# Kernel optimization log

Hardware: AMD Instinct MI355X
Metric: run time of the kernel (lower is better)

Reference implementation:

```python
import jax, jax.numpy as jnp
import numpy as np


def setup_inputs() -> dict:
    key = jax.random.key(0)
    ks = jax.random.split(key, 13)
    HID = 256
    N = 2 * HID                      # hidden_dim * 2
    B_DOC, S, T_K = 32, 40, 64      # docs, sentences/doc, max words/sentence
    B_SENT = B_DOC * S               # total sentences = sum(sent_lens)
    MAX_DOC_LEN = S * T_K
    f = jnp.float32
    sc = jnp.float32(0.05)
    sent_lens = jnp.full((B_DOC,), S, dtype=jnp.int32)
    inp = {
        "s_t_hat": jax.random.normal(ks[0], (B_DOC, N), f),
        "encoder_outputs": jax.random.normal(ks[1], (B_SENT, T_K, N), f),
        "encoder_feature": jax.random.normal(ks[2], (B_SENT * T_K, N), f) * jnp.float32(0.5),
        "seq_lens2": jax.random.randint(ks[3], (B_SENT,), T_K // 2, T_K + 1, dtype=jnp.int32),
        "sent_s_t_hat": jax.random.normal(ks[4], (B_DOC, N), f),
        "sent_enc_outputs": jax.random.normal(ks[5], (B_DOC, S, N), f),
        "sent_enc_feature": jax.random.normal(ks[6], (B_DOC * S, N), f) * jnp.float32(0.5),
        "sent_enc_padding_mask": (jnp.arange(S)[None, :] < sent_lens[:, None]).astype(f),
        "sent_lens": sent_lens,
        "max_doc_len": MAX_DOC_LEN,
        "coverage": jnp.zeros((B_SENT, T_K), f),
        "Wd": jax.random.normal(ks[7], (N, N), f) * sc,
        "bd": jax.random.normal(ks[8], (N,), f) * sc,
        "v_w": jax.random.normal(ks[9], (N,), f) * sc,
        "Wsd": jax.random.normal(ks[10], (N, N), f) * sc,
        "bsd": jax.random.normal(ks[11], (N,), f) * sc,
        "sv_w": jax.random.normal(ks[12], (N,), f) * sc,
    }
    return inp


def _excl_cumsum(x):
    return jnp.cumsum(x) - x


def reference(s_t_hat, encoder_outputs, encoder_feature, seq_lens2, sent_s_t_hat,
              sent_enc_outputs, sent_enc_feature, sent_enc_padding_mask, sent_lens,
              max_doc_len, coverage, Wd, bd, v_w, Wsd, bsd, sv_w):
    B_SENT, T_K, N = encoder_outputs.shape
    B_DOC, S, _ = sent_enc_outputs.shape
    dtype = encoder_outputs.dtype

    # sentence s -> owning doc (replaces first Python loop: broadcast dec_fea per doc)
    doc_ids = jnp.repeat(jnp.arange(B_DOC), sent_lens, total_repeat_length=B_SENT)

    # ---- word-level additive attention over each sentence ----
    dec_fea = s_t_hat @ Wd + bd                              # [B_DOC, N]
    att = jnp.tanh(encoder_feature.reshape(B_SENT, T_K, N) + dec_fea[doc_ids][:, None, :])
    scores = att @ v_w                                        # [B_SENT, T_K]
    w_mask = (jnp.arange(T_K)[None, :] < seq_lens2[:, None]).astype(dtype)
    w_attn_ = jax.nn.softmax(scores, axis=1) * w_mask
    w_attn = w_attn_ / w_attn_.sum(1, keepdims=True)          # [B_SENT, T_K]

    # ---- sentence-level additive attention over each doc ----
    sent_dec_fea = sent_s_t_hat @ Wsd + bsd                   # [B_DOC, N]
    sent_att = jnp.tanh(sent_enc_feature.reshape(B_DOC, S, N) + sent_dec_fea[:, None, :])
    sent_scores = sent_att @ sv_w                             # [B_DOC, S]
    sent_attn_ = jax.nn.softmax(sent_scores, axis=1) * sent_enc_padding_mask
    sent_attn_dist = sent_attn_ / sent_attn_.sum(1, keepdims=True)

    # ---- ragged flatten: scatter valid words of each sentence into its doc stream ----
    sent_start = _excl_cumsum(sent_lens)                      # first sentence idx per doc
    sent_local = jnp.arange(B_SENT) - sent_start[doc_ids]     # sentence pos within doc
    mult_attn = sent_attn_dist[doc_ids, sent_local][:, None] * w_attn  # [B_SENT, T_K]

    word_cum = _excl_cumsum(seq_lens2)                        # global word offsets
    doc_word_off = word_cum - word_cum[sent_start[doc_ids]]   # offset within doc
    pos = doc_word_off[:, None] + jnp.arange(T_K)[None, :]    # [B_SENT, T_K]
    valid = jnp.arange(T_K)[None, :] < seq_lens2[:, None]
    flat = jnp.where(valid, doc_ids[:, None] * max_doc_len + pos, B_DOC * max_doc_len)
    flat = flat.reshape(-1)

    enc_output2 = (jnp.zeros((B_DOC * max_doc_len, N), dtype)
                   .at[flat].set(encoder_outputs.reshape(-1, N), mode="drop")
                   .reshape(B_DOC, max_doc_len, N))
    attn_dist_sw = (jnp.zeros((B_DOC * max_doc_len,), dtype)
                    .at[flat].set(mult_attn.reshape(-1), mode="drop")
                    .reshape(B_DOC, max_doc_len))

    c_t = jnp.einsum("bl,bln->bn", attn_dist_sw, enc_output2)  # [B_DOC, N]
    return (c_t, attn_dist_sw, coverage, sent_attn_dist)
```

## Files before the change

kernel.cpp:

```cpp
#include <hip/hip_runtime.h>
#include <hip/hip_bf16.h>
#include <math.h>

#define B_DOC 32
#define S_MAX 40
#define T_K 64
#define N_DIM 512
#define B_SENT (B_DOC * S_MAX)
#define MAXDOC (S_MAX * T_K)
#define KCHUNK 4

__device__ __forceinline__ float fast_tanh(float x) {
    float e = __expf(2.0f * x);
    return 1.0f - 2.0f * __builtin_amdgcn_rcpf(e + 1.0f);
}

__global__ __launch_bounds__(256) void prep_fea_kernel(
        const int* __restrict__ seq_lens2, const int* __restrict__ sent_lens,
        const float* __restrict__ s_t_hat, const float* __restrict__ sent_s_t_hat,
        const float* __restrict__ Wd, const float* __restrict__ bd,
        const float* __restrict__ Wsd, const float* __restrict__ bsd,
        float* __restrict__ fea_part,
        int* __restrict__ doc_ids, int* __restrict__ sent_local,
        int* __restrict__ doc_word_off, int* __restrict__ sent_start_g,
        int* __restrict__ doc_words_total) {
    int tid = threadIdx.x;
    if (blockIdx.x == 256) {
        __shared__ int ss[B_DOC + 1];
        __shared__ int wc[B_SENT + 1];
        __shared__ int wsum[4];
        int lane = tid & 63, w = tid >> 6;

        int ls[5];
        #pragma unroll
        for (int k = 0; k < 5; ++k) ls[k] = seq_lens2[tid * 5 + k];
        int sum = ls[0] + ls[1] + ls[2] + ls[3] + ls[4];

        int scan = sum;
        #pragma unroll
        for (int off = 1; off < 64; off <<= 1) {
            int v = __shfl_up(scan, off, 64);
            if (lane >= off) scan += v;
        }
        if (lane == 63) wsum[w] = scan;

        if (w == 0) {
            int sl = (lane < B_DOC) ? sent_lens[lane] : 0;
            int sc2 = sl;
            #pragma unroll
            for (int off = 1; off < 64; off <<= 1) {
                int v = __shfl_up(sc2, off, 64);
                if (lane >= off) sc2 += v;
            }
            if (lane < B_DOC) ss[lane + 1] = sc2;
            if (lane == 0) ss[0] = 0;
        }
        __syncthreads();

        int wbase = 0;
        for (int i = 0; i < w; ++i) wbase += wsum[i];
        int excl = wbase + scan - sum;
        #pragma unroll
        for (int k = 0; k < 5; ++k) { wc[tid * 5 + k] = excl; excl += ls[k]; }
        if (tid == 255) wc[B_SENT] = excl;
        __syncthreads();

        if (tid <= B_DOC) sent_start_g[tid] = ss[tid];
        if (tid < B_DOC) doc_words_total[tid] = wc[ss[tid + 1]] - wc[ss[tid]];

        for (int i = tid; i < B_SENT; i += 256) {
            int lo = 0, hi = B_DOC - 1;
            while (lo < hi) { int mid = (lo + hi + 1) >> 1; if (ss[mid] <= i) lo = mid; else hi = mid - 1; }
            doc_ids[i] = lo;
            sent_local[i] = i - ss[lo];
            doc_word_off[i] = wc[i] - wc[ss[lo]];
        }
    } else {
        int blk = blockIdx.x;
        int c = blk & (KCHUNK - 1);
        int b = (blk >> 2) & 31;
        int m = blk >> 7;
        const int KC = N_DIM / KCHUNK;
        const float* x = (m ? sent_s_t_hat : s_t_hat) + b * N_DIM + c * KC;
        const float* W = (m ? Wsd : Wd) + (size_t)c * KC * N_DIM;
        const float* bias = (m ? bsd : bd);
        float* out = fea_part + ((size_t)(m * 32 + b) * KCHUNK + c) * N_DIM;
        __shared__ float xs[128];
        if (tid < KC) xs[tid] = x[tid];
        __syncthreads();
        float a0 = 0.f, a1 = 0.f;
        if (c == 0) { a0 = bias[tid]; a1 = bias[tid + 256]; }
        #pragma unroll 8
        for (int k = 0; k < KC; ++k) {
            float xv = xs[k];
            a0 = fmaf(xv, W[k * N_DIM + tid], a0);
            a1 = fmaf(xv, W[k * N_DIM + tid + 256], a1);
        }
        out[tid] = a0;
        out[tid + 256] = a1;
    }
}

__global__ __launch_bounds__(256) void sent_attn_kernel(
        const float* __restrict__ sef, const float* __restrict__ fea_part,
        const float* __restrict__ sv_w, const float* __restrict__ mask,
        float* __restrict__ out_sent) {
    int b = blockIdx.x;
    __shared__ float df[N_DIM];
    __shared__ float vw[N_DIM];
    __shared__ float sc[S_MAX];
    int tid = threadIdx.x;
    const float* fp = fea_part + (size_t)(32 + b) * KCHUNK * N_DIM;
    for (int i = tid; i < N_DIM; i += 256) {
        df[i] = fp[i] + fp[N_DIM + i] + fp[2 * N_DIM + i] + fp[3 * N_DIM + i];
        vw[i] = sv_w[i];
    }
    __syncthreads();
    int w = tid >> 6, lane = tid & 63;
    const float4* sef4 = (const float4*)(sef + (size_t)b * S_MAX * N_DIM);
    const float4* df4 = (const float4*)df;
    const float4* vw4 = (const float4*)vw;
    for (int t = w; t < S_MAX; t += 4) {
        float acc = 0.0f;
        #pragma unroll
        for (int j = 0; j < 2; ++j) {
            int n4 = lane + 64 * j;
            float4 e = sef4[t * 128 + n4];
            float4 d = df4[n4];
            float4 v = vw4[n4];
            acc = fmaf(v.x, fast_tanh(e.x + d.x), acc);
            acc = fmaf(v.y, fast_tanh(e.y + d.y), acc);
            acc = fmaf(v.z, fast_tanh(e.z + d.z), acc);
            acc = fmaf(v.w, fast_tanh(e.w + d.w), acc);
        }
        #pragma unroll
        for (int off = 32; off >= 1; off >>= 1) acc += __shfl_xor(acc, off, 64);
        if (lane == 0) sc[t] = acc;
    }
    __syncthreads();
    if (tid < 64) {
        bool valid = tid < S_MAX;
        float x = valid ? sc[tid] : -INFINITY;
        float m = x;
        #pragma unroll
        for (int off = 32; off >= 1; off >>= 1) m = fmaxf(m, __shfl_xor(m, off, 64));
        float mk = valid ? mask[b * S_MAX + tid] : 0.0f;
        float e = valid ? __expf(x - m) * mk : 0.0f;
        float ssum = e;
        #pragma unroll
        for (int off = 32; off >= 1; off >>= 1) ssum += __shfl_xor(ssum, off, 64);
        if (valid) out_sent[b * S_MAX + tid] = e / ssum;
    }
}

__global__ __launch_bounds__(256, 4) void fused_kernel(
        const float* __restrict__ ef, const float* __restrict__ eo,
        const float* __restrict__ fea_part, const float* __restrict__ v_w,
        const float* __restrict__ sent_attn, const int* __restrict__ seq_lens2,
        const int* __restrict__ doc_ids, const int* __restrict__ sent_local,
        const int* __restrict__ doc_word_off, const int* __restrict__ sent_start,
        const int* __restrict__ doc_words_total, const int* __restrict__ mdl,
        const float* __restrict__ cov_in,
        float* __restrict__ part, float* __restrict__ out_attn,
        float* __restrict__ out_cov) {
    int s = blockIdx.x;
    int tid = threadIdx.x;
    int w = tid >> 6, lane = tid & 63;
    int h = lane >> 5, sub = lane & 31;
    __shared__ float sc[T_K];
    __shared__ float wl[4];
    __shared__ __align__(16) float4 red[4][128];

    int doc = doc_ids[s];
    int len = seq_lens2[s];
    int maxdoc = mdl[0];

    const float4* fp4 = (const float4*)(fea_part + (size_t)doc * KCHUNK * N_DIM);
    const float4* vw4 = (const float4*)v_w;
    float4 d[4], v[4];
    #pragma unroll
    for (int k = 0; k < 4; ++k) {
        int j = sub + 32 * k;
        float4 a = fp4[j], b = fp4[128 + j], c = fp4[256 + j], e = fp4[384 + j];
        d[k].x = a.x + b.x + c.x + e.x;
        d[k].y = a.y + b.y + c.y + e.y;
        d[k].z = a.z + b.z + c.z + e.z;
        d[k].w = a.w + b.w + c.w + e.w;
        v[k] = vw4[j];
    }

    if (tid < T_K) out_cov[s * T_K + tid] = cov_in[s * T_K + tid];

    const float4* ef4 = (const float4*)ef + (size_t)s * T_K * 128;
    const float4* eo4 = (const float4*)eo + (size_t)s * T_K * 128;

    float l_w = 0.0f;
    float4 O[4];
    #pragma unroll
    for (int k = 0; k < 4; ++k) O[k] = (float4){0.f, 0.f, 0.f, 0.f};

    int t = 2 * w;
    float4 ea[4];
    {
        int row = t + h;
        #pragma unroll
        for (int k = 0; k < 4; ++k) ea[k] = ef4[row * 128 + sub + 32 * k];
    }
    for (; t < len; t += 8) {
        int row = t + h;
        float4 p4[4];
        #pragma unroll
        for (int k = 0; k < 4; ++k) p4[k] = eo4[row * 128 + sub + 32 * k];
        float4 eb[4];
        int tn = t + 8;
        if (tn < len) {
            int rown = tn + h;
            #pragma unroll
            for (int k = 0; k < 4; ++k) eb[k] = ef4[rown * 128 + sub + 32 * k];
        }
        float a0, a1, a2, a3;
        a0  = v[0].x * fast_tanh(ea[0].x + d[0].x);
        a1  = v[1].x * fast_tanh(ea[1].x + d[1].x);
        a2  = v[2].x * fast_tanh(ea[2].x + d[2].x);
        a3  = v[3].x * fast_tanh(ea[3].x + d[3].x);
        a0 = fmaf(v[0].y, fast_tanh(ea[0].y + d[0].y), a0);
        a1 = fmaf(v[1].y, fast_tanh(ea[1].y + d[1].y), a1);
        a2 = fmaf(v[2].y, fast_tanh(ea[2].y + d[2].y), a2);
        a3 = fmaf(v[3].y, fast_tanh(ea[3].y + d[3].y), a3);
        a0 = fmaf(v[0].z, fast_tanh(ea[0].z + d[0].z), a0);
        a1 = fmaf(v[1].z, fast_tanh(ea[1].z + d[1].z), a1);
        a2 = fmaf(v[2].z, fast_tanh(ea[2].z + d[2].z), a2);
        a3 = fmaf(v[3].z, fast_tanh(ea[3].z + d[3].z), a3);
        a0 = fmaf(v[0].w, fast_tanh(ea[0].w + d[0].w), a0);
        a1 = fmaf(v[1].w, fast_tanh(ea[1].w + d[1].w), a1);
        a2 = fmaf(v[2].w, fast_tanh(ea[2].w + d[2].w), a2);
        a3 = fmaf(v[3].w, fast_tanh(ea[3].w + d[3].w), a3);
        float acc = (a0 + a1) + (a2 + a3);
        #pragma unroll
        for (int off = 16; off >= 1; off >>= 1) acc += __shfl_xor(acc, off, 64);
        bool valid = (t + h) < len;
        if (sub == 0 && valid) sc[t + h] = acc;
        float p = valid ? __expf(acc) : 0.0f;
        l_w += p;
        #pragma unroll
        for (int k = 0; k < 4; ++k) {
            O[k].x = fmaf(p, p4[k].x, O[k].x);
            O[k].y = fmaf(p, p4[k].y, O[k].y);
            O[k].z = fmaf(p, p4[k].z, O[k].z);
            O[k].w = fmaf(p, p4[k].w, O[k].w);
        }
        #pragma unroll
        for (int k = 0; k < 4; ++k) ea[k] = eb[k];
    }

    l_w += __shfl_xor(l_w, 32, 64);
    #pragma unroll
    for (int k = 0; k < 4; ++k) {
        O[k].x += __shfl_xor(O[k].x, 32, 64);
        O[k].y += __shfl_xor(O[k].y, 32, 64);
        O[k].z += __shfl_xor(O[k].z, 32, 64);
        O[k].w += __shfl_xor(O[k].w, 32, 64);
    }
    if (lane == 0) wl[w] = l_w;
    if (h == 0) {
        #pragma unroll
        for (int k = 0; k < 4; ++k) red[w][sub + 32 * k] = O[k];
    }
    __syncthreads();

    float l = (wl[0] + wl[1]) + (wl[2] + wl[3]);
    float sa = sent_attn[doc * S_MAX + sent_local[s]];
    float inv = sa / l;
    if (tid < 128) {
        float4 a = red[0][tid], b = red[1][tid], c = red[2][tid], e = red[3][tid];
        float4 r = {(a.x + b.x + c.x + e.x) * inv, (a.y + b.y + c.y + e.y) * inv,
                    (a.z + b.z + c.z + e.z) * inv, (a.w + b.w + c.w + e.w) * inv};
        ((float4*)(part + (size_t)s * N_DIM))[tid] = r;
    }
    if (tid < T_K && tid < len) {
        float mu = sa * __expf(sc[tid]) / l;
        out_attn[(size_t)doc * maxdoc + doc_word_off[s] + tid] = mu;
    }
    if (s + 1 == sent_start[doc + 1]) {
        int dwt = doc_words_total[doc];
        for (int i = dwt + tid; i < maxdoc; i += 256)
            out_attn[(size_t)doc * maxdoc + i] = 0.0f;
    }
}

__global__ __launch_bounds__(128) void reduce_kernel(
        const float* __restrict__ part, const int* __restrict__ sent_start,
        float* __restrict__ c_t) {
    int b = blockIdx.x;
    int nq = threadIdx.x;
    int st = sent_start[b], en = sent_start[b + 1];
    float4 acc = {0.f, 0.f, 0.f, 0.f};
    for (int s = st; s < en; ++s) {
        float4 p = ((const float4*)(part + (size_t)s * N_DIM))[nq];
        acc.x += p.x; acc.y += p.y; acc.z += p.z; acc.w += p.w;
    }
    ((float4*)(c_t + (size_t)b * N_DIM))[nq] = acc;
}

extern "C" void kernel_launch(void* const* d_in, const int* in_sizes, int n_in,
                              void* d_out, int out_size, void* d_ws, size_t ws_size,
                              hipStream_t stream) {
    const float* s_t_hat        = (const float*)d_in[0];
    const float* encoder_out    = (const float*)d_in[1];
    const float* encoder_feat   = (const float*)d_in[2];
    const int*   seq_lens2      = (const int*)d_in[3];
    const float* sent_s_t_hat   = (const float*)d_in[4];
    const float* sent_enc_feat  = (const float*)d_in[6];
    const float* sent_pad_mask  = (const float*)d_in[7];
    const int*   sent_lens      = (const int*)d_in[8];
    const int*   max_doc_len    = (const int*)d_in[9];
    const float* coverage       = (const float*)d_in[10];
    const float* Wd             = (const float*)d_in[11];
    const float* bd             = (const float*)d_in[12];
    const float* v_w            = (const float*)d_in[13];
    const float* Wsd            = (const float*)d_in[14];
    const float* bsd            = (const float*)d_in[15];
    const float* sv_w           = (const float*)d_in[16];

    float* out      = (float*)d_out;
    float* o_ct     = out;
    float* o_attn   = out + B_DOC * N_DIM;
    float* o_cov    = o_attn + B_DOC * MAXDOC;
    float* o_sent   = o_cov + B_SENT * T_K;

    float* ws          = (float*)d_ws;
    float* fea_part    = ws;
    float* part        = ws + 131072;
    int*   ints        = (int*)(ws + 131072 + 655360);
    int*   doc_ids     = ints;
    int*   sent_local  = ints + B_SENT;
    int*   doc_w_off   = ints + 2 * B_SENT;
    int*   sent_start  = ints + 3 * B_SENT;
    int*   doc_wtot    = ints + 3 * B_SENT + 33;

    prep_fea_kernel<<<257, 256, 0, stream>>>(seq_lens2, sent_lens, s_t_hat,
                                             sent_s_t_hat, Wd, bd, Wsd, bsd,
                                             fea_part, doc_ids, sent_local,
                                             doc_w_off, sent_start, doc_wtot);
    sent_attn_kernel<<<B_DOC, 256, 0, stream>>>(sent_enc_feat, fea_part, sv_w,
                                                sent_pad_mask, o_sent);
    fused_kernel<<<B_SENT, 256, 0, stream>>>(encoder_feat, encoder_out, fea_part,
                                             v_w, o_sent, seq_lens2, doc_ids,
                                             sent_local, doc_w_off, sent_start,
                                             doc_wtot, max_doc_len, coverage,
                                             part, o_attn, o_cov);
    reduce_kernel<<<B_DOC, 128, 0, stream>>>(part, sent_start, o_ct);
}
```

Before: 78.04 us.

## Fuse sentence attention into stage-1 kernel and fold reduction via last-block atomics

Merges the sentence-level attention kernel into the preparation kernel: each of 32 extra blocks computes the full Wsd projection for one doc, then the sentence scores and softmax. The separate reduce kernel is removed, and the last block finishing each doc (found with an atomic counter and threadfence) sums the per-sentence partials into c_t. This cuts the launch count from four to two. In exchange, each sentence block does a serial 512-long dot loop, and every block in the main kernel now pays for a fence and an atomic.

```diff
diff --git a/kernel.cpp b/kernel.cpp
--- a/kernel.cpp
+++ b/kernel.cpp
@@ -15,21 +15,45 @@
     return 1.0f - 2.0f * __builtin_amdgcn_rcpf(e + 1.0f);
 }
 
-__global__ __launch_bounds__(256) void prep_fea_kernel(
+__global__ __launch_bounds__(256) void stage1_kernel(
         const int* __restrict__ seq_lens2, const int* __restrict__ sent_lens,
         const float* __restrict__ s_t_hat, const float* __restrict__ sent_s_t_hat,
         const float* __restrict__ Wd, const float* __restrict__ bd,
         const float* __restrict__ Wsd, const float* __restrict__ bsd,
-        float* __restrict__ fea_part,
+        const float* __restrict__ sef, const float* __restrict__ sv_w,
+        const float* __restrict__ mask,
+        float* __restrict__ fea_part, float* __restrict__ o_sent,
         int* __restrict__ doc_ids, int* __restrict__ sent_local,
         int* __restrict__ doc_word_off, int* __restrict__ sent_start_g,
-        int* __restrict__ doc_words_total) {
+        int* __restrict__ doc_words_total, int* __restrict__ cnt) {
     int tid = threadIdx.x;
-    if (blockIdx.x == 256) {
+    int blk = blockIdx.x;
+    if (blk < 128) {
+        int c = blk & (KCHUNK - 1);
+        int b = blk >> 2;
+        const int KC = N_DIM / KCHUNK;
+        const float* x = s_t_hat + b * N_DIM + c * KC;
+        const float* W = Wd + (size_t)c * KC * N_DIM;
+        float* out = fea_part + ((size_t)b * KCHUNK + c) * N_DIM;
+        __shared__ float xs[128];
+        if (tid < KC) xs[tid] = x[tid];
+        __syncthreads();
+        float a0 = 0.f, a1 = 0.f;
+        if (c == 0) { a0 = bd[tid]; a1 = bd[tid + 256]; }
+        #pragma unroll 8
+        for (int k = 0; k < KC; ++k) {
+            float xv = xs[k];
+            a0 = fmaf(xv, W[k * N_DIM + tid], a0);
+            a1 = fmaf(xv, W[k * N_DIM + tid + 256], a1);
+        }
+        out[tid] = a0;
+        out[tid + 256] = a1;
+    } else if (blk == 128) {
         __shared__ int ss[B_DOC + 1];
         __shared__ int wc[B_SENT + 1];
         __shared__ int wsum[4];
         int lane = tid & 63, w = tid >> 6;
+        if (tid < B_DOC) cnt[tid] = 0;
 
         int ls[5];
         #pragma unroll
@@ -76,80 +100,61 @@
             doc_word_off[i] = wc[i] - wc[ss[lo]];
         }
     } else {
-        int blk = blockIdx.x;
-        int c = blk & (KCHUNK - 1);
-        int b = (blk >> 2) & 31;
-        int m = blk >> 7;
-        const int KC = N_DIM / KCHUNK;
-        const float* x = (m ? sent_s_t_hat : s_t_hat) + b * N_DIM + c * KC;
-        const float* W = (m ? Wsd : Wd) + (size_t)c * KC * N_DIM;
-        const float* bias = (m ? bsd : bd);
-        float* out = fea_part + ((size_t)(m * 32 + b) * KCHUNK + c) * N_DIM;
-        __shared__ float xs[128];
-        if (tid < KC) xs[tid] = x[tid];
-        __syncthreads();
-        float a0 = 0.f, a1 = 0.f;
-        if (c == 0) { a0 = bias[tid]; a1 = bias[tid + 256]; }
+        int doc = blk - 129;
+        __shared__ __align__(16) float xs[N_DIM];
+        __shared__ __align__(16) float df[N_DIM];
+        __shared__ __align__(16) float vw[N_DIM];
+        __shared__ float sc[S_MAX];
+        xs[tid] = sent_s_t_hat[doc * N_DIM + tid];
+        xs[tid + 256] = sent_s_t_hat[doc * N_DIM + tid + 256];
+        vw[tid] = sv_w[tid];
+        vw[tid + 256] = sv_w[tid + 256];
+        __syncthreads();
+        float a0 = bsd[tid], a1 = bsd[tid + 256];
         #pragma unroll 8
-        for (int k = 0; k < KC; ++k) {
+        for (int k = 0; k < N_DIM; ++k) {
             float xv = xs[k];
-            a0 = fmaf(xv, W[k * N_DIM + tid], a0);
-            a1 = fmaf(xv, W[k * N_DIM + tid + 256], a1);
-        }
-        out[tid] = a0;
-        out[tid + 256] = a1;
-    }
-}
-
-__global__ __launch_bounds__(256) void sent_attn_kernel(
-        const float* __restrict__ sef, const float* __restrict__ fea_part,
-        const float* __restrict__ sv_w, const float* __restrict__ mask,
-        float* __restrict__ out_sent) {
-    int b = blockIdx.x;
-    __shared__ float df[N_DIM];
-    __shared__ float vw[N_DIM];
-    __shared__ float sc[S_MAX];
-    int tid = threadIdx.x;
-    const float* fp = fea_part + (size_t)(32 + b) * KCHUNK * N_DIM;
-    for (int i = tid; i < N_DIM; i += 256) {
-        df[i] = fp[i] + fp[N_DIM + i] + fp[2 * N_DIM + i] + fp[3 * N_DIM + i];
-        vw[i] = sv_w[i];
-    }
-    __syncthreads();
-    int w = tid >> 6, lane = tid & 63;
-    const float4* sef4 = (const float4*)(sef + (size_t)b * S_MAX * N_DIM);
-    const float4* df4 = (const float4*)df;
-    const float4* vw4 = (const float4*)vw;
-    for (int t = w; t < S_MAX; t += 4) {
-        float acc = 0.0f;
-        #pragma unroll
-        for (int j = 0; j < 2; ++j) {
-            int n4 = lane + 64 * j;
-            float4 e = sef4[t * 128 + n4];
-            float4 d = df4[n4];
-            float4 v = vw4[n4];
-            acc = fmaf(v.x, fast_tanh(e.x + d.x), acc);
-            acc = fmaf(v.y, fast_tanh(e.y + d.y), acc);
-            acc = fmaf(v.z, fast_tanh(e.z + d.z), acc);
-            acc = fmaf(v.w, fast_tanh(e.w + d.w), acc);
-        }
-        #pragma unroll
-        for (int off = 32; off >= 1; off >>= 1) acc += __shfl_xor(acc, off, 64);
-        if (lane == 0) sc[t] = acc;
-    }
-    __syncthreads();
-    if (tid < 64) {
-        bool valid = tid < S_MAX;
-        float x = valid ? sc[tid] : -INFINITY;
-        float m = x;
-        #pragma unroll
-        for (int off = 32; off >= 1; off >>= 1) m = fmaxf(m, __shfl_xor(m, off, 64));
-        float mk = valid ? mask[b * S_MAX + tid] : 0.0f;
-        float e = valid ? __expf(x - m) * mk : 0.0f;
-        float ssum = e;
-        #pragma unroll
-        for (int off = 32; off >= 1; off >>= 1) ssum += __shfl_xor(ssum, off, 64);
-        if (valid) out_sent[b * S_MAX + tid] = e / ssum;
+            a0 = fmaf(xv, Wsd[k * N_DIM + tid], a0);
+            a1 = fmaf(xv, Wsd[k * N_DIM + tid + 256], a1);
+        }
+        df[tid] = a0;
+        df[tid + 256] = a1;
+        __syncthreads();
+        int g = tid >> 5, sub = tid & 31;
+        const float4* df4 = (const float4*)df;
+        const float4* vw4 = (const float4*)vw;
+        for (int r = g; r < S_MAX; r += 8) {
+            const float4* row = (const float4*)(sef + ((size_t)doc * S_MAX + r) * N_DIM);
+            float acc = 0.0f;
+            #pragma unroll
+            for (int k = 0; k < 4; ++k) {
+                int j = sub + 32 * k;
+                float4 e = row[j];
+                float4 d = df4[j];
+                float4 v = vw4[j];
+                acc = fmaf(v.x, fast_tanh(e.x + d.x), acc);
+                acc = fmaf(v.y, fast_tanh(e.y + d.y), acc);
+                acc = fmaf(v.z, fast_tanh(e.z + d.z), acc);
+                acc = fmaf(v.w, fast_tanh(e.w + d.w), acc);
+            }
+            #pragma unroll
+            for (int off = 16; off >= 1; off >>= 1) acc += __shfl_xor(acc, off, 32);
+            if (sub == 0) sc[r] = acc;
+        }
+        __syncthreads();
+        if (tid < 64) {
+            bool valid = tid < S_MAX;
+            float x = valid ? sc[tid] : -INFINITY;
+            float m = x;
+            #pragma unroll
+            for (int off = 32; off >= 1; off >>= 1) m = fmaxf(m, __shfl_xor(m, off, 64));
+            float mk = valid ? mask[doc * S_MAX + tid] : 0.0f;
+            float e = valid ? __expf(x - m) * mk : 0.0f;
+            float ssum = e;
+            #pragma unroll
+            for (int off = 32; off >= 1; off >>= 1) ssum += __shfl_xor(ssum, off, 64);
+            if (valid) o_sent[doc * S_MAX + tid] = e / ssum;
+        }
     }
 }
 
@@ -162,7 +167,8 @@
         const int* __restrict__ doc_words_total, const int* __restrict__ mdl,
         const float* __restrict__ cov_in,
         float* __restrict__ part, float* __restrict__ out_attn,
-        float* __restrict__ out_cov) {
+        float* __restrict__ out_cov, float* __restrict__ c_t,
+        int* __restrict__ cnt) {
     int s = blockIdx.x;
     int tid = threadIdx.x;
     int w = tid >> 6, lane = tid & 63;
@@ -170,6 +176,7 @@
     __shared__ float sc[T_K];
     __shared__ float wl[4];
     __shared__ __align__(16) float4 red[4][128];
+    __shared__ int isLast;
 
     int doc = doc_ids[s];
     int len = seq_lens2[s];
@@ -281,25 +288,30 @@
         float mu = sa * __expf(sc[tid]) / l;
         out_attn[(size_t)doc * maxdoc + doc_word_off[s] + tid] = mu;
     }
-    if (s + 1 == sent_start[doc + 1]) {
+    int st = sent_start[doc], en = sent_start[doc + 1];
+    if (s + 1 == en) {
         int dwt = doc_words_total[doc];
         for (int i = dwt + tid; i < maxdoc; i += 256)
             out_attn[(size_t)doc * maxdoc + i] = 0.0f;
     }
-}
-
-__global__ __launch_bounds__(128) void reduce_kernel(
-        const float* __restrict__ part, const int* __restrict__ sent_start,
-        float* __restrict__ c_t) {
-    int b = blockIdx.x;
-    int nq = threadIdx.x;
-    int st = sent_start[b], en = sent_start[b + 1];
-    float4 acc = {0.f, 0.f, 0.f, 0.f};
-    for (int s = st; s < en; ++s) {
-        float4 p = ((const float4*)(part + (size_t)s * N_DIM))[nq];
-        acc.x += p.x; acc.y += p.y; acc.z += p.z; acc.w += p.w;
-    }
-    ((float4*)(c_t + (size_t)b * N_DIM))[nq] = acc;
+
+    __threadfence();
+    if (tid == 0) {
+        int old = atomicAdd(&cnt[doc], 1);
+        isLast = (old == (en - st) - 1);
+    }
+    __syncthreads();
+    if (isLast) {
+        __threadfence();
+        if (tid < 128) {
+            float4 acc = {0.f, 0.f, 0.f, 0.f};
+            for (int r = st; r < en; ++r) {
+                float4 p = ((const float4*)(part + (size_t)r * N_DIM))[tid];
+                acc.x += p.x; acc.y += p.y; acc.z += p.z; acc.w += p.w;
+            }
+            ((float4*)(c_t + (size_t)doc * N_DIM))[tid] = acc;
+        }
+    }
 }
 
 extern "C" void kernel_launch(void* const* d_in, const int* in_sizes, int n_in,
@@ -330,24 +342,23 @@
 
     float* ws          = (float*)d_ws;
     float* fea_part    = ws;
-    float* part        = ws + 131072;
-    int*   ints        = (int*)(ws + 131072 + 655360);
+    float* part        = ws + 65536;
+    int*   ints        = (int*)(ws + 65536 + 655360);
     int*   doc_ids     = ints;
     int*   sent_local  = ints + B_SENT;
     int*   doc_w_off   = ints + 2 * B_SENT;
     int*   sent_start  = ints + 3 * B_SENT;
     int*   doc_wtot    = ints + 3 * B_SENT + 33;
-
-    prep_fea_kernel<<<257, 256, 0, stream>>>(seq_lens2, sent_lens, s_t_hat,
-                                             sent_s_t_hat, Wd, bd, Wsd, bsd,
-                                             fea_part, doc_ids, sent_local,
-                                             doc_w_off, sent_start, doc_wtot);
-    sent_attn_kernel<<<B_DOC, 256, 0, stream>>>(sent_enc_feat, fea_part, sv_w,
-                                                sent_pad_mask, o_sent);
+    int*   cnt         = ints + 3 * B_SENT + 65;
+
+    stage1_kernel<<<161, 256, 0, stream>>>(seq_lens2, sent_lens, s_t_hat,
+                                           sent_s_t_hat, Wd, bd, Wsd, bsd,
+                                           sent_enc_feat, sv_w, sent_pad_mask,
+                                           fea_part, o_sent, doc_ids, sent_local,
+                                           doc_w_off, sent_start, doc_wtot, cnt);
     fused_kernel<<<B_SENT, 256, 0, stream>>>(encoder_feat, encoder_out, fea_part,
                                              v_w, o_sent, seq_lens2, doc_ids,
                                              sent_local, doc_w_off, sent_start,
                                              doc_wtot, max_doc_len, coverage,
-                                             part, o_attn, o_cov);
-    reduce_kernel<<<B_DOC, 128, 0, stream>>>(part, sent_start, o_ct);
+                                             part, o_attn, o_cov, o_ct, cnt);
 }
```

After: 300.5 us. 3.85x slower.

## Fold sentence attention into word kernel blocks and defer scaling to finalize

Applied to the files above, without the earlier changes.

Removes the separate sentence-attention launch by adding extra blocks to the word-level kernel that compute sentence softmax. Word kernel now writes unscaled normalized weights to a workspace buffer, and a new finalize kernel applies sentence attention scaling to both the context reduction and the scattered attention output. This cuts one launch and removes the dependency of the big kernel on the sentence kernel, at the cost of an extra workspace write/read of word weights and heavier per-doc finalize work.

```diff
diff --git a/kernel.cpp b/kernel.cpp
--- a/kernel.cpp
+++ b/kernel.cpp
@@ -101,71 +101,66 @@
     }
 }
 
-__global__ __launch_bounds__(256) void sent_attn_kernel(
-        const float* __restrict__ sef, const float* __restrict__ fea_part,
-        const float* __restrict__ sv_w, const float* __restrict__ mask,
-        float* __restrict__ out_sent) {
-    int b = blockIdx.x;
-    __shared__ float df[N_DIM];
-    __shared__ float vw[N_DIM];
-    __shared__ float sc[S_MAX];
-    int tid = threadIdx.x;
-    const float* fp = fea_part + (size_t)(32 + b) * KCHUNK * N_DIM;
-    for (int i = tid; i < N_DIM; i += 256) {
-        df[i] = fp[i] + fp[N_DIM + i] + fp[2 * N_DIM + i] + fp[3 * N_DIM + i];
-        vw[i] = sv_w[i];
-    }
-    __syncthreads();
-    int w = tid >> 6, lane = tid & 63;
-    const float4* sef4 = (const float4*)(sef + (size_t)b * S_MAX * N_DIM);
-    const float4* df4 = (const float4*)df;
-    const float4* vw4 = (const float4*)vw;
-    for (int t = w; t < S_MAX; t += 4) {
-        float acc = 0.0f;
-        #pragma unroll
-        for (int j = 0; j < 2; ++j) {
-            int n4 = lane + 64 * j;
-            float4 e = sef4[t * 128 + n4];
-            float4 d = df4[n4];
-            float4 v = vw4[n4];
-            acc = fmaf(v.x, fast_tanh(e.x + d.x), acc);
-            acc = fmaf(v.y, fast_tanh(e.y + d.y), acc);
-            acc = fmaf(v.z, fast_tanh(e.z + d.z), acc);
-            acc = fmaf(v.w, fast_tanh(e.w + d.w), acc);
-        }
-        #pragma unroll
-        for (int off = 32; off >= 1; off >>= 1) acc += __shfl_xor(acc, off, 64);
-        if (lane == 0) sc[t] = acc;
-    }
-    __syncthreads();
-    if (tid < 64) {
-        bool valid = tid < S_MAX;
-        float x = valid ? sc[tid] : -INFINITY;
-        float m = x;
-        #pragma unroll
-        for (int off = 32; off >= 1; off >>= 1) m = fmaxf(m, __shfl_xor(m, off, 64));
-        float mk = valid ? mask[b * S_MAX + tid] : 0.0f;
-        float e = valid ? __expf(x - m) * mk : 0.0f;
-        float ssum = e;
-        #pragma unroll
-        for (int off = 32; off >= 1; off >>= 1) ssum += __shfl_xor(ssum, off, 64);
-        if (valid) out_sent[b * S_MAX + tid] = e / ssum;
-    }
-}
-
 __global__ __launch_bounds__(256, 4) void fused_kernel(
         const float* __restrict__ ef, const float* __restrict__ eo,
-        const float* __restrict__ fea_part, const float* __restrict__ v_w,
-        const float* __restrict__ sent_attn, const int* __restrict__ seq_lens2,
-        const int* __restrict__ doc_ids, const int* __restrict__ sent_local,
-        const int* __restrict__ doc_word_off, const int* __restrict__ sent_start,
-        const int* __restrict__ doc_words_total, const int* __restrict__ mdl,
-        const float* __restrict__ cov_in,
-        float* __restrict__ part, float* __restrict__ out_attn,
-        float* __restrict__ out_cov) {
+        const float* __restrict__ sef, const float* __restrict__ fea_part,
+        const float* __restrict__ v_w, const float* __restrict__ sv_w,
+        const float* __restrict__ mask, const int* __restrict__ seq_lens2,
+        const int* __restrict__ doc_ids, const float* __restrict__ cov_in,
+        float* __restrict__ part, float* __restrict__ wn,
+        float* __restrict__ out_cov, float* __restrict__ o_sent) {
     int s = blockIdx.x;
     int tid = threadIdx.x;
     int w = tid >> 6, lane = tid & 63;
+
+    if (s >= B_SENT) {
+        int doc = s - B_SENT;
+        __shared__ __align__(16) float df[N_DIM];
+        __shared__ __align__(16) float vw[N_DIM];
+        __shared__ float sc2[S_MAX];
+        const float* fp = fea_part + (size_t)(32 + doc) * KCHUNK * N_DIM;
+        for (int i = tid; i < N_DIM; i += 256) {
+            df[i] = fp[i] + fp[N_DIM + i] + fp[2 * N_DIM + i] + fp[3 * N_DIM + i];
+            vw[i] = sv_w[i];
+        }
+        __syncthreads();
+        const float4* sef4 = (const float4*)(sef + (size_t)doc * S_MAX * N_DIM);
+        const float4* df4 = (const float4*)df;
+        const float4* vw4 = (const float4*)vw;
+        for (int t = w; t < S_MAX; t += 4) {
+            float acc = 0.0f;
+            #pragma unroll
+            for (int j = 0; j < 2; ++j) {
+                int n4 = lane + 64 * j;
+                float4 e = sef4[t * 128 + n4];
+                float4 d = df4[n4];
+                float4 v = vw4[n4];
+                acc = fmaf(v.x, fast_tanh(e.x + d.x), acc);
+                acc = fmaf(v.y, fast_tanh(e.y + d.y), acc);
+                acc = fmaf(v.z, fast_tanh(e.z + d.z), acc);
+                acc = fmaf(v.w, fast_tanh(e.w + d.w), acc);
+            }
+            #pragma unroll
+            for (int off = 32; off >= 1; off >>= 1) acc += __shfl_xor(acc, off, 64);
+            if (lane == 0) sc2[t] = acc;
+        }
+        __syncthreads();
+        if (tid < 64) {
+            bool valid = tid < S_MAX;
+            float x = valid ? sc2[tid] : -INFINITY;
+            float m = x;
+            #pragma unroll
+            for (int off = 32; off >= 1; off >>= 1) m = fmaxf(m, __shfl_xor(m, off, 64));
+            float mk = valid ? mask[doc * S_MAX + tid] : 0.0f;
+            float e = valid ? __expf(x - m) * mk : 0.0f;
+            float ssum = e;
+            #pragma unroll
+            for (int off = 32; off >= 1; off >>= 1) ssum += __shfl_xor(ssum, off, 64);
+            if (valid) o_sent[doc * S_MAX + tid] = e / ssum;
+        }
+        return;
+    }
+
     int h = lane >> 5, sub = lane & 31;
     __shared__ float sc[T_K];
     __shared__ float wl[4];
@@ -173,7 +168,6 @@
 
     int doc = doc_ids[s];
     int len = seq_lens2[s];
-    int maxdoc = mdl[0];
 
     const float4* fp4 = (const float4*)(fea_part + (size_t)doc * KCHUNK * N_DIM);
     const float4* vw4 = (const float4*)v_w;
@@ -269,37 +263,56 @@
     __syncthreads();
 
     float l = (wl[0] + wl[1]) + (wl[2] + wl[3]);
-    float sa = sent_attn[doc * S_MAX + sent_local[s]];
-    float inv = sa / l;
+    float inv = 1.0f / l;
     if (tid < 128) {
         float4 a = red[0][tid], b = red[1][tid], c = red[2][tid], e = red[3][tid];
         float4 r = {(a.x + b.x + c.x + e.x) * inv, (a.y + b.y + c.y + e.y) * inv,
                     (a.z + b.z + c.z + e.z) * inv, (a.w + b.w + c.w + e.w) * inv};
         ((float4*)(part + (size_t)s * N_DIM))[tid] = r;
     }
-    if (tid < T_K && tid < len) {
-        float mu = sa * __expf(sc[tid]) / l;
-        out_attn[(size_t)doc * maxdoc + doc_word_off[s] + tid] = mu;
-    }
-    if (s + 1 == sent_start[doc + 1]) {
-        int dwt = doc_words_total[doc];
-        for (int i = dwt + tid; i < maxdoc; i += 256)
-            out_attn[(size_t)doc * maxdoc + i] = 0.0f;
-    }
-}
-
-__global__ __launch_bounds__(128) void reduce_kernel(
-        const float* __restrict__ part, const int* __restrict__ sent_start,
-        float* __restrict__ c_t) {
-    int b = blockIdx.x;
-    int nq = threadIdx.x;
-    int st = sent_start[b], en = sent_start[b + 1];
-    float4 acc = {0.f, 0.f, 0.f, 0.f};
-    for (int s = st; s < en; ++s) {
-        float4 p = ((const float4*)(part + (size_t)s * N_DIM))[nq];
-        acc.x += p.x; acc.y += p.y; acc.z += p.z; acc.w += p.w;
-    }
-    ((float4*)(c_t + (size_t)b * N_DIM))[nq] = acc;
+    if (tid < T_K && tid < len) wn[s * T_K + tid] = __expf(sc[tid]) * inv;
+}
+
+__global__ __launch_bounds__(256) void finalize_kernel(
+        const float* __restrict__ part, const float* __restrict__ wn,
+        const float* __restrict__ o_sent, const int* __restrict__ seq_lens2,
+        const int* __restrict__ sent_start, const int* __restrict__ doc_word_off,
+        const int* __restrict__ doc_words_total, const int* __restrict__ mdl,
+        float* __restrict__ c_t, float* __restrict__ out_attn) {
+    int doc = blockIdx.x;
+    int tid = threadIdx.x;
+    int maxdoc = mdl[0];
+    __shared__ float sa_sh[S_MAX];
+    int st = sent_start[doc], en = sent_start[doc + 1];
+    int ns = en - st;
+    if (tid < S_MAX) sa_sh[tid] = o_sent[doc * S_MAX + tid];
+    __syncthreads();
+
+    if (tid < 128) {
+        float4 acc = {0.f, 0.f, 0.f, 0.f};
+        for (int i = 0; i < ns; ++i) {
+            float sa = sa_sh[i];
+            float4 p = ((const float4*)(part + (size_t)(st + i) * N_DIM))[tid];
+            acc.x = fmaf(sa, p.x, acc.x);
+            acc.y = fmaf(sa, p.y, acc.y);
+            acc.z = fmaf(sa, p.z, acc.z);
+            acc.w = fmaf(sa, p.w, acc.w);
+        }
+        ((float4*)(c_t + (size_t)doc * N_DIM))[tid] = acc;
+    }
+
+    int w = tid >> 6, lane = tid & 63;
+    for (int i = w; i < ns; i += 4) {
+        int s = st + i;
+        int len = seq_lens2[s];
+        float sa = sa_sh[i];
+        if (lane < len)
+            out_attn[(size_t)doc * maxdoc + doc_word_off[s] + lane] =
+                sa * wn[s * T_K + lane];
+    }
+    int dwt = doc_words_total[doc];
+    for (int i = dwt + tid; i < maxdoc; i += 256)
+        out_attn[(size_t)doc * maxdoc + i] = 0.0f;
 }
 
 extern "C" void kernel_launch(void* const* d_in, const int* in_sizes, int n_in,
@@ -331,7 +344,8 @@
     float* ws          = (float*)d_ws;
     float* fea_part    = ws;
     float* part        = ws + 131072;
-    int*   ints        = (int*)(ws + 131072 + 655360);
+    float* wn          = ws + 131072 + 655360;
+    int*   ints        = (int*)(ws + 131072 + 655360 + 81920);
     int*   doc_ids     = ints;
     int*   sent_local  = ints + B_SENT;
     int*   doc_w_off   = ints + 2 * B_SENT;
@@ -342,12 +356,12 @@
                                              sent_s_t_hat, Wd, bd, Wsd, bsd,
                                              fea_part, doc_ids, sent_local,
                                              doc_w_off, sent_start, doc_wtot);
-    sent_attn_kernel<<<B_DOC, 256, 0, stream>>>(sent_enc_feat, fea_part, sv_w,
-                                                sent_pad_mask, o_sent);
-    fused_kernel<<<B_SENT, 256, 0, stream>>>(encoder_feat, encoder_out, fea_part,
-                                             v_w, o_sent, seq_lens2, doc_ids,
-                                             sent_local, doc_w_off, sent_start,
-                                             doc_wtot, max_doc_len, coverage,
-                                             part, o_attn, o_cov);
-    reduce_kernel<<<B_DOC, 128, 0, stream>>>(part, sent_start, o_ct);
-}
+    fused_kernel<<<B_SENT + B_DOC, 256, 0, stream>>>(encoder_feat, encoder_out,
+                                                     sent_enc_feat, fea_part,
+                                                     v_w, sv_w, sent_pad_mask,
+                                                     seq_lens2, doc_ids, coverage,
+                                                     part, wn, o_cov, o_sent);
+    finalize_kernel<<<B_DOC, 256, 0, stream>>>(part, wn, o_sent, seq_lens2,
+                                               sent_start, doc_w_off, doc_wtot,
+                                               max_doc_len, o_ct, o_attn);
+}
```

After: 67.62 us (median of 2 runs). 1.15x faster.
